# Kernel tuning notes

Measured on AMD Instinct MI355X. Metric: run time of the kernel, lower is better.

## Reference

```python
import jax, jax.numpy as jnp
import numpy as np

SEQ, H, NC = 20, 128, 100000

def _lstm_cell(x, h, c, Wih, Whh, bih, bhh):
    # gates: [B, 4H] in PyTorch order i, f, g, o
    g = x @ Wih.T + bih + h @ Whh.T + bhh
    i, f, gg, o = jnp.split(g, 4, axis=-1)
    c2 = jax.nn.sigmoid(f) * c + jax.nn.sigmoid(i) * jnp.tanh(gg)
    h2 = jax.nn.sigmoid(o) * jnp.tanh(c2)
    return h2, c2

def setup_inputs() -> dict:
    key = jax.random.key(0)
    ks = jax.random.split(key, 24)
    u = lambda k, shp, bound: jax.random.uniform(k, shp, jnp.float32, -bound, bound)
    s1 = 1.0 / np.sqrt(H)       # PyTorch LSTMCell init bound, hidden_size=H
    s2 = 1.0 / np.sqrt(2 * H)   # combined cell, hidden_size=2H
    kn = lambda k, shp: jax.random.normal(k, shp, jnp.float32) * np.sqrt(2.0 / shp[1])  # kaiming_normal_
    return {
        'x': jax.random.normal(ks[0], (SEQ, 1, H), jnp.float32),
        'h0f': kn(ks[1], (1, H)), 'c0f': kn(ks[2], (1, H)),
        'h0b': kn(ks[3], (1, H)), 'c0b': kn(ks[4], (1, H)),
        'h0l': kn(ks[5], (1, 2 * H)), 'c0l': kn(ks[6], (1, 2 * H)),
        'Wih_f': u(ks[7], (4 * H, H), s1), 'Whh_f': u(ks[8], (4 * H, H), s1),
        'bih_f': u(ks[9], (4 * H,), s1), 'bhh_f': u(ks[10], (4 * H,), s1),
        'Wih_b': u(ks[11], (4 * H, H), s1), 'Whh_b': u(ks[12], (4 * H, H), s1),
        'bih_b': u(ks[13], (4 * H,), s1), 'bhh_b': u(ks[14], (4 * H,), s1),
        'Wih_l': u(ks[15], (8 * H, 2 * H), s2), 'Whh_l': u(ks[16], (8 * H, 2 * H), s2),
        'bih_l': u(ks[17], (8 * H,), s2), 'bhh_l': u(ks[18], (8 * H,), s2),
        'Wlin': u(ks[19], (NC, 2 * H), 1.0 / np.sqrt(2 * H)),
        'blin': u(ks[20], (NC,), 1.0 / np.sqrt(2 * H)),
    }

def reference(x, h0f, c0f, h0b, c0b, h0l, c0l,
              Wih_f, Whh_f, bih_f, bhh_f,
              Wih_b, Whh_b, bih_b, bhh_b,
              Wih_l, Whh_l, bih_l, bhh_l,
              Wlin, blin):
    xs = x.reshape(SEQ, 1, H)

    def step_f(carry, xt):
        h, c = _lstm_cell(xt, carry[0], carry[1], Wih_f, Whh_f, bih_f, bhh_f)
        return (h, c), h
    _, fwd = jax.lax.scan(step_f, (h0f, c0f), xs)          # [SEQ, 1, H]

    def step_b(carry, xt):
        h, c = _lstm_cell(xt, carry[0], carry[1], Wih_b, Whh_b, bih_b, bhh_b)
        return (h, c), h
    # backward list is kept in reversed-scan order (NOT flipped back), per source zip
    _, bwd = jax.lax.scan(step_b, (h0b, c0b), xs[::-1])    # [SEQ, 1, H]

    comb = jnp.concatenate([fwd, bwd], axis=-1)            # [SEQ, 1, 2H]

    def step_l(carry, xt):
        h, c = _lstm_cell(xt, carry[0], carry[1], Wih_l, Whh_l, bih_l, bhh_l)
        return (h, c), h
    _, hl = jax.lax.scan(step_l, (h0l, c0l), comb)         # [SEQ, 1, 2H]

    fb = hl.reshape(SEQ, 2 * H)
    return fb @ Wlin.T + blin                              # [SEQ, NC]
```

## Files before the change

kernel.cpp:

```cpp
#include <hip/hip_runtime.h>
#include <stdint.h>

#define SEQ  20
#define H1   128
#define H2   256
#define NCLS 100000

__device__ __forceinline__ float sigm(float x) { return 1.0f / (1.0f + __expf(-x)); }
__device__ __forceinline__ float tanhfast(float x) {
    float e = __expf(-2.0f * fabsf(x));
    float t = (1.0f - e) / (1.0f + e);
    return copysignf(t, x);
}

__device__ __forceinline__ void gbar(int* cnt, int target) {
    __syncthreads();
    if (threadIdx.x == 0) {
        __hip_atomic_fetch_add(cnt, 1, __ATOMIC_ACQ_REL, __HIP_MEMORY_SCOPE_AGENT);
        while (__hip_atomic_load(cnt, __ATOMIC_ACQUIRE, __HIP_MEMORY_SCOPE_AGENT) < target)
            __builtin_amdgcn_s_sleep(1);
    }
    __syncthreads();
}

__global__ __launch_bounds__(512, 2) void k_l1r(
    const float* __restrict__ x,
    const float* __restrict__ h0f, const float* __restrict__ c0f,
    const float* __restrict__ h0b, const float* __restrict__ c0b,
    const float* __restrict__ WihF, const float* __restrict__ WhhF,
    const float* __restrict__ bihF, const float* __restrict__ bhhF,
    const float* __restrict__ WihB, const float* __restrict__ WhhB,
    const float* __restrict__ bihB, const float* __restrict__ bhhB,
    float* __restrict__ comb)
{
    const int dir = blockIdx.x;
    const float* Wih = dir ? WihB : WihF;
    const float* Whh = dir ? WhhB : WhhF;
    const float* bih = dir ? bihB : bihF;
    const float* bhh = dir ? bhhB : bhhF;
    const float* h0  = dir ? h0b  : h0f;
    const float* c0  = dir ? c0b  : c0f;

    __shared__ float xs[SEQ * H1];
    __shared__ float hcur[H1];
    __shared__ float gv[4 * H1];
    __shared__ float gxs[4 * H1][SEQ + 1];

    const int tid = threadIdx.x;

    for (int i = tid; i < SEQ * H1; i += 512) xs[i] = x[i];
    if (tid < H1) hcur[tid] = h0[tid];
    float creg = (tid < H1) ? c0[tid] : 0.0f;
    const float bias = bih[tid] + bhh[tid];

    float w[H1];
    {
        const float* wr = Wih + tid * H1;
#pragma unroll
        for (int k = 0; k < H1; k += 4) {
            float4 v = *(const float4*)(wr + k);
            w[k] = v.x; w[k + 1] = v.y; w[k + 2] = v.z; w[k + 3] = v.w;
        }
    }
    __syncthreads();

    for (int t = 0; t < SEQ; ++t) {
        const float* xp = xs + (dir ? (SEQ - 1 - t) : t) * H1;
        float a0 = 0.f, a1 = 0.f, a2 = 0.f, a3 = 0.f;
#pragma unroll
        for (int k = 0; k < H1; k += 4) {
            float4 hv = *(const float4*)(xp + k);
            a0 += w[k] * hv.x; a1 += w[k + 1] * hv.y;
            a2 += w[k + 2] * hv.z; a3 += w[k + 3] * hv.w;
        }
        gxs[tid][t] = bias + ((a0 + a1) + (a2 + a3));
    }

    {
        const float* wr = Whh + tid * H1;
#pragma unroll
        for (int k = 0; k < H1; k += 4) {
            float4 v = *(const float4*)(wr + k);
            w[k] = v.x; w[k + 1] = v.y; w[k + 2] = v.z; w[k + 3] = v.w;
        }
    }

    for (int t = 0; t < SEQ; ++t) {
        float a0 = 0.f, a1 = 0.f, a2 = 0.f, a3 = 0.f;
#pragma unroll
        for (int k = 0; k < H1; k += 4) {
            float4 hv = *(const float4*)(hcur + k);
            a0 += w[k] * hv.x; a1 += w[k + 1] * hv.y;
            a2 += w[k + 2] * hv.z; a3 += w[k + 3] * hv.w;
        }
        gv[tid] = gxs[tid][t] + ((a0 + a1) + (a2 + a3));
        __syncthreads();
        if (tid < H1) {
            float gi = gv[tid], gf = gv[H1 + tid], gg = gv[2 * H1 + tid], go = gv[3 * H1 + tid];
            float cn = sigm(gf) * creg + sigm(gi) * tanhfast(gg);
            creg = cn;
            float hn = sigm(go) * tanhfast(cn);
            comb[t * H2 + dir * H1 + tid] = hn;
            hcur[tid] = hn;
        }
        __syncthreads();
    }
}

__global__ __launch_bounds__(512, 2) void k_l2r(
    const float* __restrict__ Whhl,
    const float* __restrict__ h0l, const float* __restrict__ c0l,
    const float* __restrict__ Wihl,
    const float* __restrict__ bihl, const float* __restrict__ bhhl,
    const float* __restrict__ comb,
    float* __restrict__ fb,
    float* __restrict__ hg2,
    int* __restrict__ sync)
{
    const int b = blockIdx.x;
    __shared__ float cs[SEQ * H2];
    __shared__ float hcur[H2];
    __shared__ float gv[4 * 64];
    __shared__ float gxs[H2][SEQ + 1];

    const int tid  = threadIdx.x;
    const int L    = tid >> 1;
    const int half = tid & 1;
    const int R    = (L >> 6) * H2 + b * 64 + (L & 63);
    const float bias = bihl[R] + bhhl[R];

    for (int i = tid; i < SEQ * H2; i += 512) cs[i] = comb[i];
    if (tid < H2) hcur[tid] = h0l[tid];
    float creg = (tid < 64) ? c0l[b * 64 + tid] : 0.0f;

    float w[H1];
    {
        const float* wr = Wihl + R * H2 + half * H1;
#pragma unroll
        for (int k = 0; k < H1; k += 4) {
            float4 v = *(const float4*)(wr + k);
            w[k] = v.x; w[k + 1] = v.y; w[k + 2] = v.z; w[k + 3] = v.w;
        }
    }
    __syncthreads();

    for (int t = 0; t < SEQ; ++t) {
        const float* cp = cs + t * H2 + half * H1;
        float a0 = 0.f, a1 = 0.f, a2 = 0.f, a3 = 0.f;
#pragma unroll
        for (int k = 0; k < H1; k += 4) {
            float4 hv = *(const float4*)(cp + k);
            a0 += w[k] * hv.x; a1 += w[k + 1] * hv.y;
            a2 += w[k + 2] * hv.z; a3 += w[k + 3] * hv.w;
        }
        float a = (a0 + a1) + (a2 + a3);
        a += __shfl_xor(a, 1);
        if (half == 0) gxs[L][t] = bias + a;
    }

    {
        const float* wr = Whhl + R * H2 + half * H1;
#pragma unroll
        for (int k = 0; k < H1; k += 4) {
            float4 v = *(const float4*)(wr + k);
            w[k] = v.x; w[k + 1] = v.y; w[k + 2] = v.z; w[k + 3] = v.w;
        }
    }

    for (int t = 0; t < SEQ; ++t) {
        const float* hp = hcur + half * H1;
        float a0 = 0.f, a1 = 0.f, a2 = 0.f, a3 = 0.f;
#pragma unroll
        for (int k = 0; k < H1; k += 4) {
            float4 hv = *(const float4*)(hp + k);
            a0 += w[k] * hv.x; a1 += w[k + 1] * hv.y;
            a2 += w[k + 2] * hv.z; a3 += w[k + 3] * hv.w;
        }
        float a = (a0 + a1) + (a2 + a3);
        a += __shfl_xor(a, 1);
        if (half == 0) gv[L] = gxs[L][t] + a;
        __syncthreads();
        if (tid < 64) {
            float gi = gv[tid], gf = gv[64 + tid], gg = gv[128 + tid], go = gv[192 + tid];
            float cn = sigm(gf) * creg + sigm(gi) * tanhfast(gg);
            creg = cn;
            float hn = sigm(go) * tanhfast(cn);
            fb[t * H2 + b * 64 + tid] = hn;
            __hip_atomic_store(&hg2[b * 64 + tid], hn,
                               __ATOMIC_RELEASE, __HIP_MEMORY_SCOPE_AGENT);
        }
        gbar(&sync[0], 4 * (t + 1));
        if (tid < H2)
            hcur[tid] = __hip_atomic_load(&hg2[tid],
                                          __ATOMIC_RELAXED, __HIP_MEMORY_SCOPE_AGENT);
        __syncthreads();
    }
}

__global__ __launch_bounds__(256, 4) void k_out_v(
    const float* __restrict__ Wlin, const float* __restrict__ blin,
    const float* __restrict__ fb, float* __restrict__ out)
{
    __shared__ float fbs[H2][SEQ];
    const int tid = threadIdx.x;
    for (int t = 0; t < SEQ; ++t) fbs[tid][t] = fb[t * H2 + tid];
    __syncthreads();

    int n = blockIdx.x * 256 + tid;
    if (n >= NCLS) return;
    float acc[SEQ];
    float bv = blin[n];
#pragma unroll
    for (int t = 0; t < SEQ; ++t) acc[t] = bv;

    const float* wp = Wlin + (size_t)n * H2;
    for (int k = 0; k < H2; k += 4) {
        float4 wv = *(const float4*)(wp + k);
#pragma unroll
        for (int t = 0; t < SEQ; t += 4) {
            float4 f0 = *(const float4*)(&fbs[k][t]);
            float4 f1 = *(const float4*)(&fbs[k + 1][t]);
            float4 f2 = *(const float4*)(&fbs[k + 2][t]);
            float4 f3 = *(const float4*)(&fbs[k + 3][t]);
            acc[t]     += wv.x * f0.x + wv.y * f1.x + wv.z * f2.x + wv.w * f3.x;
            acc[t + 1] += wv.x * f0.y + wv.y * f1.y + wv.z * f2.y + wv.w * f3.y;
            acc[t + 2] += wv.x * f0.z + wv.y * f1.z + wv.z * f2.z + wv.w * f3.z;
            acc[t + 3] += wv.x * f0.w + wv.y * f1.w + wv.z * f2.w + wv.w * f3.w;
        }
    }
#pragma unroll
    for (int t = 0; t < SEQ; ++t)
        out[(size_t)t * NCLS + n] = acc[t];
}

extern "C" void kernel_launch(void* const* d_in, const int* in_sizes, int n_in,
                              void* d_out, int out_size, void* d_ws, size_t ws_size,
                              hipStream_t stream)
{
    const float* x    = (const float*)d_in[0];
    const float* h0f_ = (const float*)d_in[1];
    const float* c0f_ = (const float*)d_in[2];
    const float* h0b_ = (const float*)d_in[3];
    const float* c0b_ = (const float*)d_in[4];
    const float* h0l_ = (const float*)d_in[5];
    const float* c0l_ = (const float*)d_in[6];
    const float* WihF = (const float*)d_in[7];
    const float* WhhF = (const float*)d_in[8];
    const float* bihF = (const float*)d_in[9];
    const float* bhhF = (const float*)d_in[10];
    const float* WihB = (const float*)d_in[11];
    const float* WhhB = (const float*)d_in[12];
    const float* bihB = (const float*)d_in[13];
    const float* bhhB = (const float*)d_in[14];
    const float* Wihl = (const float*)d_in[15];
    const float* Whhl = (const float*)d_in[16];
    const float* bihl = (const float*)d_in[17];
    const float* bhhl = (const float*)d_in[18];
    const float* Wlin = (const float*)d_in[19];
    const float* blin = (const float*)d_in[20];

    char* ws = (char*)d_ws;
    int*   sync = (int*)ws;
    float* hg2  = (float*)(ws + 1536);
    float* comb = (float*)(ws + 4096);
    float* fb   = (float*)(ws + 24576);

    hipMemsetAsync(sync, 0, 256, stream);

    k_l1r<<<2, 512, 0, stream>>>(x, h0f_, c0f_, h0b_, c0b_,
                                 WihF, WhhF, bihF, bhhF,
                                 WihB, WhhB, bihB, bhhB,
                                 comb);
    k_l2r<<<4, 512, 0, stream>>>(Whhl, h0l_, c0l_,
                                 Wihl, bihl, bhhl,
                                 comb, fb, hg2, sync);
    k_out_v<<<391, 256, 0, stream>>>(Wlin, blin, fb, (float*)d_out);
}
```

Before: 397.8 us.

## Split LSTM matvecs across 1024 threads and replace grid barrier with per-block flags

Both recurrent kernels now run with 1024 threads. Each thread computes two gate rows over a 32-column slice, and the partial sums are reduced through shared memory, which shortens the serial dot-product chain per step. In layer 2, the atomic-counter grid barrier is replaced by per-block step flags: each block publishes its hidden slice and waits only on the producers it needs, and its own slice is written to shared memory directly. The cost is an extra shared-memory reduction and extra __syncthreads per step, and per-thread register use drops from 128 weights to 64.

New measurement: 354.3 us. 10.9% less time.

```diff
diff --git a/kernel.cpp b/kernel.cpp
--- a/kernel.cpp
+++ b/kernel.cpp
@@ -13,17 +13,7 @@
     return copysignf(t, x);
 }
 
-__device__ __forceinline__ void gbar(int* cnt, int target) {
-    __syncthreads();
-    if (threadIdx.x == 0) {
-        __hip_atomic_fetch_add(cnt, 1, __ATOMIC_ACQ_REL, __HIP_MEMORY_SCOPE_AGENT);
-        while (__hip_atomic_load(cnt, __ATOMIC_ACQUIRE, __HIP_MEMORY_SCOPE_AGENT) < target)
-            __builtin_amdgcn_s_sleep(1);
-    }
-    __syncthreads();
-}
-
-__global__ __launch_bounds__(512, 2) void k_l1r(
+__global__ __launch_bounds__(1024, 4) void k_l1(
     const float* __restrict__ x,
     const float* __restrict__ h0f, const float* __restrict__ c0f,
     const float* __restrict__ h0b, const float* __restrict__ c0b,
@@ -43,71 +33,87 @@
 
     __shared__ float xs[SEQ * H1];
     __shared__ float hcur[H1];
-    __shared__ float gv[4 * H1];
+    __shared__ float biasL[4 * H1];
     __shared__ float gxs[4 * H1][SEQ + 1];
+    __shared__ float partial[4 * 520];
 
     const int tid = threadIdx.x;
-
-    for (int i = tid; i < SEQ * H1; i += 512) xs[i] = x[i];
+    const int cg  = tid >> 8;
+    const int rp  = tid & 255;
+    const int r0  = rp * 2;
+
+    for (int i = tid; i < SEQ * H1; i += 1024) xs[i] = x[i];
+    if (tid < 4 * H1) biasL[tid] = bih[tid] + bhh[tid];
     if (tid < H1) hcur[tid] = h0[tid];
     float creg = (tid < H1) ? c0[tid] : 0.0f;
-    const float bias = bih[tid] + bhh[tid];
-
-    float w[H1];
+
+    float4 wa[8], wb[8];
     {
-        const float* wr = Wih + tid * H1;
-#pragma unroll
-        for (int k = 0; k < H1; k += 4) {
-            float4 v = *(const float4*)(wr + k);
-            w[k] = v.x; w[k + 1] = v.y; w[k + 2] = v.z; w[k + 3] = v.w;
-        }
+        const float4* pa = (const float4*)(Wih + r0 * H1 + cg * 32);
+        const float4* pb = (const float4*)(Wih + (r0 + 1) * H1 + cg * 32);
+#pragma unroll
+        for (int j = 0; j < 8; ++j) { wa[j] = pa[j]; wb[j] = pb[j]; }
     }
     __syncthreads();
 
     for (int t = 0; t < SEQ; ++t) {
-        const float* xp = xs + (dir ? (SEQ - 1 - t) : t) * H1;
-        float a0 = 0.f, a1 = 0.f, a2 = 0.f, a3 = 0.f;
-#pragma unroll
-        for (int k = 0; k < H1; k += 4) {
-            float4 hv = *(const float4*)(xp + k);
-            a0 += w[k] * hv.x; a1 += w[k + 1] * hv.y;
-            a2 += w[k + 2] * hv.z; a3 += w[k + 3] * hv.w;
-        }
-        gxs[tid][t] = bias + ((a0 + a1) + (a2 + a3));
+        const float4* xp = (const float4*)(xs + (dir ? (SEQ - 1 - t) : t) * H1 + cg * 32);
+        float a0 = 0.f, a1 = 0.f;
+#pragma unroll
+        for (int j = 0; j < 8; ++j) {
+            float4 v = xp[j];
+            a0 += wa[j].x * v.x + wa[j].y * v.y + wa[j].z * v.z + wa[j].w * v.w;
+            a1 += wb[j].x * v.x + wb[j].y * v.y + wb[j].z * v.z + wb[j].w * v.w;
+        }
+        *(float2*)(partial + cg * 520 + r0) = make_float2(a0, a1);
+        __syncthreads();
+        if (tid < 4 * H1) {
+            float s = biasL[tid] + partial[tid] + partial[520 + tid]
+                    + partial[1040 + tid] + partial[1560 + tid];
+            gxs[tid][t] = s;
+        }
+        __syncthreads();
     }
 
     {
-        const float* wr = Whh + tid * H1;
-#pragma unroll
-        for (int k = 0; k < H1; k += 4) {
-            float4 v = *(const float4*)(wr + k);
-            w[k] = v.x; w[k + 1] = v.y; w[k + 2] = v.z; w[k + 3] = v.w;
-        }
+        const float4* pa = (const float4*)(Whh + r0 * H1 + cg * 32);
+        const float4* pb = (const float4*)(Whh + (r0 + 1) * H1 + cg * 32);
+#pragma unroll
+        for (int j = 0; j < 8; ++j) { wa[j] = pa[j]; wb[j] = pb[j]; }
     }
 
     for (int t = 0; t < SEQ; ++t) {
-        float a0 = 0.f, a1 = 0.f, a2 = 0.f, a3 = 0.f;
-#pragma unroll
-        for (int k = 0; k < H1; k += 4) {
-            float4 hv = *(const float4*)(hcur + k);
-            a0 += w[k] * hv.x; a1 += w[k + 1] * hv.y;
-            a2 += w[k + 2] * hv.z; a3 += w[k + 3] * hv.w;
-        }
-        gv[tid] = gxs[tid][t] + ((a0 + a1) + (a2 + a3));
+        const float4* hp = (const float4*)(hcur + cg * 32);
+        float a0 = 0.f, a1 = 0.f;
+#pragma unroll
+        for (int j = 0; j < 8; ++j) {
+            float4 v = hp[j];
+            a0 += wa[j].x * v.x + wa[j].y * v.y + wa[j].z * v.z + wa[j].w * v.w;
+            a1 += wb[j].x * v.x + wb[j].y * v.y + wb[j].z * v.z + wb[j].w * v.w;
+        }
+        *(float2*)(partial + cg * 520 + r0) = make_float2(a0, a1);
         __syncthreads();
         if (tid < H1) {
-            float gi = gv[tid], gf = gv[H1 + tid], gg = gv[2 * H1 + tid], go = gv[3 * H1 + tid];
-            float cn = sigm(gf) * creg + sigm(gi) * tanhfast(gg);
+            const int c = tid;
+            float s[4];
+#pragma unroll
+            for (int g = 0; g < 4; ++g) {
+                float acc = gxs[g * H1 + c][t];
+#pragma unroll
+                for (int q = 0; q < 4; ++q) acc += partial[q * 520 + g * H1 + c];
+                s[g] = acc;
+            }
+            float cn = sigm(s[1]) * creg + sigm(s[0]) * tanhfast(s[2]);
             creg = cn;
-            float hn = sigm(go) * tanhfast(cn);
-            comb[t * H2 + dir * H1 + tid] = hn;
-            hcur[tid] = hn;
-        }
-        __syncthreads();
-    }
-}
-
-__global__ __launch_bounds__(512, 2) void k_l2r(
+            float hn = sigm(s[3]) * tanhfast(cn);
+            comb[t * H2 + dir * H1 + c] = hn;
+            hcur[c] = hn;
+        }
+        __syncthreads();
+    }
+}
+
+__global__ __launch_bounds__(1024, 4) void k_l2(
     const float* __restrict__ Whhl,
     const float* __restrict__ h0l, const float* __restrict__ c0l,
     const float* __restrict__ Wihl,
@@ -115,84 +121,110 @@
     const float* __restrict__ comb,
     float* __restrict__ fb,
     float* __restrict__ hg2,
-    int* __restrict__ sync)
+    int* __restrict__ flags)
 {
     const int b = blockIdx.x;
     __shared__ float cs[SEQ * H2];
     __shared__ float hcur[H2];
-    __shared__ float gv[4 * 64];
+    __shared__ float biasL[H2];
     __shared__ float gxs[H2][SEQ + 1];
-
-    const int tid  = threadIdx.x;
-    const int L    = tid >> 1;
-    const int half = tid & 1;
-    const int R    = (L >> 6) * H2 + b * 64 + (L & 63);
-    const float bias = bihl[R] + bhhl[R];
-
-    for (int i = tid; i < SEQ * H2; i += 512) cs[i] = comb[i];
-    if (tid < H2) hcur[tid] = h0l[tid];
+    __shared__ float partial[8 * 260];
+
+    const int tid = threadIdx.x;
+    const int cg  = tid >> 7;
+    const int rp  = tid & 127;
+    const int L0  = rp * 2;
+    const int R0  = (L0 >> 6) * H2 + b * 64 + (L0 & 63);
+
+    for (int i = tid; i < SEQ * H2; i += 1024) cs[i] = comb[i];
+    if (tid < H2) {
+        int g = tid >> 6, c = tid & 63;
+        int R = g * H2 + b * 64 + c;
+        biasL[tid] = bihl[R] + bhhl[R];
+        hcur[tid]  = h0l[tid];
+    }
     float creg = (tid < 64) ? c0l[b * 64 + tid] : 0.0f;
 
-    float w[H1];
+    float4 wa[8], wb[8];
     {
-        const float* wr = Wihl + R * H2 + half * H1;
-#pragma unroll
-        for (int k = 0; k < H1; k += 4) {
-            float4 v = *(const float4*)(wr + k);
-            w[k] = v.x; w[k + 1] = v.y; w[k + 2] = v.z; w[k + 3] = v.w;
-        }
+        const float4* pa = (const float4*)(Wihl + (size_t)R0 * H2 + cg * 32);
+        const float4* pb = (const float4*)(Wihl + (size_t)(R0 + 1) * H2 + cg * 32);
+#pragma unroll
+        for (int j = 0; j < 8; ++j) { wa[j] = pa[j]; wb[j] = pb[j]; }
     }
     __syncthreads();
 
     for (int t = 0; t < SEQ; ++t) {
-        const float* cp = cs + t * H2 + half * H1;
-        float a0 = 0.f, a1 = 0.f, a2 = 0.f, a3 = 0.f;
-#pragma unroll
-        for (int k = 0; k < H1; k += 4) {
-            float4 hv = *(const float4*)(cp + k);
-            a0 += w[k] * hv.x; a1 += w[k + 1] * hv.y;
-            a2 += w[k + 2] * hv.z; a3 += w[k + 3] * hv.w;
-        }
-        float a = (a0 + a1) + (a2 + a3);
-        a += __shfl_xor(a, 1);
-        if (half == 0) gxs[L][t] = bias + a;
+        const float4* cp = (const float4*)(cs + t * H2 + cg * 32);
+        float a0 = 0.f, a1 = 0.f;
+#pragma unroll
+        for (int j = 0; j < 8; ++j) {
+            float4 v = cp[j];
+            a0 += wa[j].x * v.x + wa[j].y * v.y + wa[j].z * v.z + wa[j].w * v.w;
+            a1 += wb[j].x * v.x + wb[j].y * v.y + wb[j].z * v.z + wb[j].w * v.w;
+        }
+        *(float2*)(partial + cg * 260 + L0) = make_float2(a0, a1);
+        __syncthreads();
+        if (tid < H2) {
+            float s = biasL[tid];
+#pragma unroll
+            for (int q = 0; q < 8; ++q) s += partial[q * 260 + tid];
+            gxs[tid][t] = s;
+        }
+        __syncthreads();
     }
 
     {
-        const float* wr = Whhl + R * H2 + half * H1;
-#pragma unroll
-        for (int k = 0; k < H1; k += 4) {
-            float4 v = *(const float4*)(wr + k);
-            w[k] = v.x; w[k + 1] = v.y; w[k + 2] = v.z; w[k + 3] = v.w;
-        }
+        const float4* pa = (const float4*)(Whhl + (size_t)R0 * H2 + cg * 32);
+        const float4* pb = (const float4*)(Whhl + (size_t)(R0 + 1) * H2 + cg * 32);
+#pragma unroll
+        for (int j = 0; j < 8; ++j) { wa[j] = pa[j]; wb[j] = pb[j]; }
     }
 
     for (int t = 0; t < SEQ; ++t) {
-        const float* hp = hcur + half * H1;
-        float a0 = 0.f, a1 = 0.f, a2 = 0.f, a3 = 0.f;
-#pragma unroll
-        for (int k = 0; k < H1; k += 4) {
-            float4 hv = *(const float4*)(hp + k);
-            a0 += w[k] * hv.x; a1 += w[k + 1] * hv.y;
-            a2 += w[k + 2] * hv.z; a3 += w[k + 3] * hv.w;
-        }
-        float a = (a0 + a1) + (a2 + a3);
-        a += __shfl_xor(a, 1);
-        if (half == 0) gv[L] = gxs[L][t] + a;
-        __syncthreads();
+        const float4* hp = (const float4*)(hcur + cg * 32);
+        float a0 = 0.f, a1 = 0.f;
+#pragma unroll
+        for (int j = 0; j < 8; ++j) {
+            float4 v = hp[j];
+            a0 += wa[j].x * v.x + wa[j].y * v.y + wa[j].z * v.z + wa[j].w * v.w;
+            a1 += wb[j].x * v.x + wb[j].y * v.y + wb[j].z * v.z + wb[j].w * v.w;
+        }
+        *(float2*)(partial + cg * 260 + L0) = make_float2(a0, a1);
+        __syncthreads();
+
         if (tid < 64) {
-            float gi = gv[tid], gf = gv[64 + tid], gg = gv[128 + tid], go = gv[192 + tid];
-            float cn = sigm(gf) * creg + sigm(gi) * tanhfast(gg);
+            const int c = tid;
+            float s[4];
+#pragma unroll
+            for (int g = 0; g < 4; ++g) {
+                float acc = gxs[g * 64 + c][t];
+#pragma unroll
+                for (int q = 0; q < 8; ++q) acc += partial[q * 260 + g * 64 + c];
+                s[g] = acc;
+            }
+            float cn = sigm(s[1]) * creg + sigm(s[0]) * tanhfast(s[2]);
             creg = cn;
-            float hn = sigm(go) * tanhfast(cn);
-            fb[t * H2 + b * 64 + tid] = hn;
-            __hip_atomic_store(&hg2[b * 64 + tid], hn,
-                               __ATOMIC_RELEASE, __HIP_MEMORY_SCOPE_AGENT);
-        }
-        gbar(&sync[0], 4 * (t + 1));
-        if (tid < H2)
-            hcur[tid] = __hip_atomic_load(&hg2[tid],
+            float hn = sigm(s[3]) * tanhfast(cn);
+            fb[t * H2 + b * 64 + c] = hn;
+            hcur[b * 64 + c] = hn;
+            if (t + 1 < SEQ) {
+                __hip_atomic_store(&hg2[b * 64 + c], hn,
+                                   __ATOMIC_RELAXED, __HIP_MEMORY_SCOPE_AGENT);
+                __threadfence();
+                if (tid == 0)
+                    __hip_atomic_store(&flags[b], t + 1,
+                                       __ATOMIC_RELEASE, __HIP_MEMORY_SCOPE_AGENT);
+            }
+        } else if (tid < 256 && t + 1 < SEQ) {
+            const int idx = (b * 64 + tid) & 255;
+            const int sh  = idx >> 6;
+            while (__hip_atomic_load(&flags[sh], __ATOMIC_ACQUIRE,
+                                     __HIP_MEMORY_SCOPE_AGENT) <= t)
+                __builtin_amdgcn_s_sleep(1);
+            hcur[idx] = __hip_atomic_load(&hg2[idx],
                                           __ATOMIC_RELAXED, __HIP_MEMORY_SCOPE_AGENT);
+        }
         __syncthreads();
     }
 }
@@ -260,19 +292,19 @@
     const float* blin = (const float*)d_in[20];
 
     char* ws = (char*)d_ws;
-    int*   sync = (int*)ws;
-    float* hg2  = (float*)(ws + 1536);
-    float* comb = (float*)(ws + 4096);
-    float* fb   = (float*)(ws + 24576);
-
-    hipMemsetAsync(sync, 0, 256, stream);
-
-    k_l1r<<<2, 512, 0, stream>>>(x, h0f_, c0f_, h0b_, c0b_,
+    int*   flags = (int*)ws;
+    float* hg2   = (float*)(ws + 1536);
+    float* comb  = (float*)(ws + 4096);
+    float* fb    = (float*)(ws + 24576);
+
+    hipMemsetAsync(flags, 0, 256, stream);
+
+    k_l1<<<2, 1024, 0, stream>>>(x, h0f_, c0f_, h0b_, c0b_,
                                  WihF, WhhF, bihF, bhhF,
                                  WihB, WhhB, bihB, bhhB,
                                  comb);
-    k_l2r<<<4, 512, 0, stream>>>(Whhl, h0l_, c0l_,
+    k_l2<<<4, 1024, 0, stream>>>(Whhl, h0l_, c0l_,
                                  Wihl, bihl, bhhl,
-                                 comb, fb, hg2, sync);
+                                 comb, fb, hg2, flags);
     k_out_v<<<391, 256, 0, stream>>>(Wlin, blin, fb, (float*)d_out);
 }
```
